# Kernel tuning notes

Hardware: AMD Instinct MI355X
Metric: run time of the kernel (lower is better)

## Reference

```python
import jax, jax.numpy as jnp
import numpy as np
from jax import lax

RATIOS = (0.5, 1.0, 2.0)
SCALES = (8, 16, 32)
BASE = 16
STRIDE = 16
N_PRE = 6000
N_POST = 300      # post-NMS proposals kept
NMS_THRESH = 0.7
MIN_SIZE = 16.0


def _anchor_base():
    x = y = BASE / 2.0
    ab = np.zeros((len(RATIOS) * len(SCALES), 4), np.float32)
    for i, r in enumerate(RATIOS):
        for j, s in enumerate(SCALES):
            h = BASE * s * np.sqrt(r)
            w = BASE * s * np.sqrt(1.0 / r)
            k = i * len(SCALES) + j
            ab[k] = [y - h / 2, x - w / 2, y + h / 2, x + w / 2]
    return ab


def _anchors(h, w):
    ab = _anchor_base()
    sy = np.arange(0, h * STRIDE, STRIDE)
    sx = np.arange(0, w * STRIDE, STRIDE)
    sx, sy = np.meshgrid(sx, sy)
    shift = np.stack((sy.ravel(), sx.ravel(), sy.ravel(), sx.ravel()), axis=1)
    # [K, A, 4] -> [K*A, 4], row-major over (y, x) pixels matching NHWC flatten
    return (ab[None, :, :] + shift[:, None, :]).reshape(-1, 4).astype(np.float32)


def _conv(x, w, b, pad):
    y = lax.conv_general_dilated(x, w, (1, 1), ((pad, pad), (pad, pad)),
                                 dimension_numbers=('NCHW', 'OIHW', 'NCHW'))
    return y + b[None, :, None, None]


def _loc2bbox(anchor, loc):
    h = anchor[:, 2] - anchor[:, 0]
    w = anchor[:, 3] - anchor[:, 1]
    cy = anchor[:, 0] + 0.5 * h
    cx = anchor[:, 1] + 0.5 * w
    dy, dx, dh, dw = loc[:, 0], loc[:, 1], loc[:, 2], loc[:, 3]
    ncy = dy * h + cy
    ncx = dx * w + cx
    nh = jnp.exp(dh) * h
    nw = jnp.exp(dw) * w
    return jnp.stack([ncy - 0.5 * nh, ncx - 0.5 * nw, ncy + 0.5 * nh, ncx + 0.5 * nw], axis=1)


def _iou(b):
    tl = jnp.maximum(b[:, None, :2], b[None, :, :2])
    br = jnp.minimum(b[:, None, 2:], b[None, :, 2:])
    wh = jnp.clip(br - tl, 0.0)
    inter = wh[..., 0] * wh[..., 1]
    area = (b[:, 2] - b[:, 0]) * (b[:, 3] - b[:, 1])
    return inter / (area[:, None] + area[None, :] - inter + 1e-9)


def _nms_keep(iou):
    # greedy NMS over score-sorted boxes: suppress later boxes overlapping kept earlier ones
    n = iou.shape[0]
    idx = jnp.arange(n)
    def step(keep, i):
        sup = (iou[i] > NMS_THRESH) & (idx > i) & keep[i]
        return keep & (~sup), None
    keep, _ = lax.scan(step, jnp.ones((n,), dtype=bool), idx)
    return keep


def _proposal(loc, fg, anchor, img_h, img_w, scale=1.0):
    boxes = _loc2bbox(anchor, loc)
    boxes = jnp.stack([jnp.clip(boxes[:, 0], 0.0, img_h),
                       jnp.clip(boxes[:, 1], 0.0, img_w),
                       jnp.clip(boxes[:, 2], 0.0, img_h),
                       jnp.clip(boxes[:, 3], 0.0, img_w)], axis=1)
    hs = boxes[:, 2] - boxes[:, 0]
    ws = boxes[:, 3] - boxes[:, 1]
    ms = MIN_SIZE * scale
    score = jnp.where((hs >= ms) & (ws >= ms), fg, -jnp.inf)
    top, idx = lax.top_k(score, N_PRE)
    bk = boxes[idx]                                    # [N_PRE, 4]
    keep = _nms_keep(_iou(lax.stop_gradient(bk)))      # selection is non-differentiable
    fs = jnp.where(keep, top, -jnp.inf)
    _, o2 = lax.top_k(fs, N_POST)
    return bk[o2]                                      # [N_POST, 4]


def setup_inputs() -> dict:
    key = jax.random.key(0)
    ks = jax.random.split(key, 4)
    C, H, W = 512, 50, 76
    return {
        "feature": jax.random.normal(ks[0], (1, C, H, W), jnp.float32),
        "conv1_w": jax.random.normal(ks[1], (512, C, 3, 3), jnp.float32) * 0.01,
        "conv1_b": jnp.zeros((512,), jnp.float32),
        "score_w": jax.random.normal(ks[2], (18, 512, 1, 1), jnp.float32) * 0.01,
        "score_b": jnp.zeros((18,), jnp.float32),
        "loc_w": jax.random.normal(ks[3], (36, 512, 1, 1), jnp.float32) * 0.01,
        "loc_b": jnp.zeros((36,), jnp.float32),
        "img_h": 800,
        "img_w": 1216,
    }


def reference(feature, conv1_w, conv1_b, score_w, score_b, loc_w, loc_b, img_h, img_w):
    _, c, h, w = feature.shape
    A = 9
    anchor = jnp.asarray(_anchors(h, w))
    x = jax.nn.relu(_conv(feature, conv1_w, conv1_b, 1))
    locs = _conv(x, loc_w, loc_b, 0)
    rpn_locs = locs.transpose(0, 2, 3, 1).reshape(1, -1, 4)
    sc = _conv(x, score_w, score_b, 0).transpose(0, 2, 3, 1)   # [1, h, w, 2A]
    sm = jax.nn.softmax(sc.reshape(1, h, w, A, 2), axis=-1)
    fg = sm[..., 1].reshape(-1)
    rpn_scores = sc.reshape(1, -1, 2)
    rois = _proposal(rpn_locs[0], fg, anchor, float(img_h), float(img_w), scale=1.0)
    return rpn_locs, rpn_scores, rois, anchor
```

## Files before the change

kernel.cpp:

```cpp
#include <hip/hip_runtime.h>

#define HH 50
#define WW2 76
#define NPIX 3800
#define CIN 512
#define NANCH 34200
#define NPRE 6000
#define NPOST 300
#define WPR 94

typedef unsigned long long u64;
typedef unsigned int u32;

__device__ __forceinline__ int PADL(int i) { return i + (i >> 4); }

template <bool DOW>
__global__ __launch_bounds__(256) void rpn_wtrans(const float* __restrict__ wgt,
                                                  float* __restrict__ wt,
                                                  const float* __restrict__ sw,
                                                  const float* __restrict__ lw,
                                                  float* __restrict__ wt2,
                                                  u32* __restrict__ hist,
                                                  u32* __restrict__ info) {
    __shared__ float tile[32][33];
    const int bx = blockIdx.x;
    const int by = blockIdx.y;
    const int t  = threadIdx.x;
    const int tx = t & 31, ty = t >> 5;
    int gid = (by * 144 + bx) * 256 + t;
    if (gid < 65536) hist[gid] = 0u;
    else if (gid < 65552) info[gid - 65536] = 0u;
    if (gid < 32768) {
        int c = gid >> 6, n = gid & 63;
        float v = 0.f;
        if (n < 18) v = sw[n * 512 + c];
        else if (n < 54) v = lw[(n - 18) * 512 + c];
        wt2[((c >> 2) * 64 + n) * 4 + (c & 3)] = v;
    }
    if (!DOW) return;
#pragma unroll
    for (int r = 0; r < 32; r += 8) {
        int ko = by * 32 + ty + r;
        tile[ty + r][tx] = wgt[(size_t)ko * 4608 + bx * 32 + tx];
    }
    __syncthreads();
#pragma unroll
    for (int r = 0; r < 32; r += 8) {
        int cit = bx * 32 + ty + r;
        wt[(size_t)cit * 512 + by * 32 + tx] = tile[tx][ty + r];
    }
}

template <bool USEWT>
__global__ __launch_bounds__(256, 2) void rpn_conv1(
    const float* __restrict__ feat, const float* __restrict__ wsrc,
    float* __restrict__ Xpt, int cin_blk, int czbase) {
    const int yb = blockIdx.x;
    const int kg = blockIdx.y;
    const int cz = blockIdx.z + czbase;
    const int t  = threadIdx.x;
    const int kp = t & 15;
    const int ty = t >> 4;
    const int row  = ty >> 2;
    const int xseg = ty & 3;
    const int x0 = xseg * 19;
    __shared__ float in_l[2048];
    __shared__ float w_l[2304];

    const int y0 = yb * 4 - 1;
    int inSrc[8]; u32 inValid = 0, inPad = 0;
#pragma unroll
    for (int k = 0; k < 8; ++k) {
        int q = t + k * 256;
        int c = q / 504, rem = q - c * 504;
        int r = rem / 84, xx = rem - r * 84;
        int gy = y0 + r, gx = xx - 1;
        bool inb = q < 2016;
        bool ok = inb && ((unsigned)gy < 50u) && ((unsigned)gx < 76u);
        inSrc[k] = c * NPIX + gy * 76 + gx;
        if (ok) inValid |= (1u << k);
        else if (inb) inPad |= (1u << k);
    }
#pragma unroll
    for (int k = 0; k < 8; ++k)
        if ((inPad >> k) & 1) in_l[t + k * 256] = 0.f;

    const float* wb;
    int wOffA = 0;
    int wSrc[9];
    if (USEWT) {
        wb = wsrc + (size_t)(cz * cin_blk) * 9 * 512 + kg * 64;
        wOffA = 8 * t - 7 * (t & 63);
    } else {
        wb = wsrc + (size_t)(kg * 64) * 4608 + (size_t)(cz * cin_blk) * 9;
#pragma unroll
        for (int k = 0; k < 9; ++k) {
            int q = t + k * 256;
            int c = q / 576, r2 = q - c * 576;
            int tap = r2 >> 6, ko = r2 & 63;
            wSrc[k] = ko * 4608 + c * 9 + tap;
        }
    }

    const float* fb = feat + (size_t)(cz * cin_blk) * NPIX;
    float acc[4][19];
#pragma unroll
    for (int o = 0; o < 4; ++o)
#pragma unroll
        for (int p = 0; p < 19; ++p) acc[o][p] = 0.f;

    const int niter = cin_blk >> 2;
#pragma unroll 1
    for (int it = 0; it < niter; ++it) {
        __syncthreads();
#pragma unroll
        for (int k = 0; k < 8; ++k)
            if ((inValid >> k) & 1) in_l[t + k * 256] = fb[inSrc[k]];
        if (USEWT) {
#pragma unroll
            for (int k = 0; k < 9; ++k)
                w_l[t + k * 256] = wb[wOffA + k * 2048];
        } else {
#pragma unroll
            for (int k = 0; k < 9; ++k)
                w_l[t + k * 256] = wb[wSrc[k]];
        }
        __syncthreads();
#pragma unroll 1
        for (int c = 0; c < 4; ++c) {
            const float* ir0 = &in_l[(c * 6 + row) * 84 + x0];
            const float* wl  = &w_l[c * 576 + 4 * kp];
#pragma unroll
            for (int r = 0; r < 3; ++r) {
                const float* ir = ir0 + r * 84;
                float win[21];
#pragma unroll
                for (int w = 0; w < 21; ++w) win[w] = ir[w];
                float wv[4][3];
#pragma unroll
                for (int tp = 0; tp < 3; ++tp) {
                    const float* wr = wl + (r * 3 + tp) * 64;
#pragma unroll
                    for (int o = 0; o < 4; ++o) wv[o][tp] = wr[o];
                }
#pragma unroll
                for (int p = 0; p < 19; ++p) {
#pragma unroll
                    for (int o = 0; o < 4; ++o) {
                        acc[o][p] = fmaf(wv[o][0], win[p],     acc[o][p]);
                        acc[o][p] = fmaf(wv[o][1], win[p + 1], acc[o][p]);
                        acc[o][p] = fmaf(wv[o][2], win[p + 2], acc[o][p]);
                    }
                }
            }
        }
        fb += 4 * NPIX;
        wb += USEWT ? 4 * 9 * 512 : 36;
    }

    const int k0 = kg * 64 + 4 * kp;
    const int y = yb * 4 + row;
    if (y < 50) {
        float* d0 = Xpt + ((size_t)cz * NPIX + y * 76 + x0) * 512 + k0;
#pragma unroll
        for (int p = 0; p < 19; ++p)
            *reinterpret_cast<float4*>(d0 + (size_t)p * 512) =
                make_float4(acc[0][p], acc[1][p], acc[2][p], acc[3][p]);
    }
}

__global__ __launch_bounds__(256) void rpn_head(
    const float* __restrict__ Xpt, const float* __restrict__ wt2,
    const float* __restrict__ b1,
    const float* __restrict__ sb, const float* __restrict__ lb,
    const int* __restrict__ ihp, const int* __restrict__ iwp,
    float* __restrict__ out, float* __restrict__ boxes,
    u32* __restrict__ keys, u32* __restrict__ hist, int nz) {
    const int p0 = blockIdx.x * 8;
    const int t  = threadIdx.x;
    __shared__ __align__(16) float xs[8 * 512];
    __shared__ float ovl[8][64];
    float4* dst = reinterpret_cast<float4*>(xs);
#pragma unroll
    for (int i = 0; i < 4; ++i) {
        int idx = t + i * 256;
        int px = idx >> 7, cc = idx & 127;
        float4 v = *reinterpret_cast<const float4*>(b1 + cc * 4);
        const float* src = Xpt + ((size_t)(p0 + px)) * 512 + cc * 4;
        for (int z = 0; z < nz; ++z) {
            float4 x = *reinterpret_cast<const float4*>(src + (size_t)z * NPIX * 512);
            v.x += x.x; v.y += x.y; v.z += x.z; v.w += x.w;
        }
        v.x = fmaxf(v.x, 0.f); v.y = fmaxf(v.y, 0.f);
        v.z = fmaxf(v.z, 0.f); v.w = fmaxf(v.w, 0.f);
        dst[idx] = v;
    }
    __syncthreads();
    const int w = t >> 6, lane = t & 63;
    float a0, a1;
    {
        float b = (lane < 18) ? sb[lane] : ((lane < 54) ? lb[lane - 18] : 0.f);
        a0 = b; a1 = b;
    }
    const float4* wv = reinterpret_cast<const float4*>(wt2) + lane;
    const float* x0b = xs + (2 * w) * 512;
    const float* x1b = xs + (2 * w + 1) * 512;
#pragma unroll 4
    for (int c4 = 0; c4 < 128; ++c4) {
        float4 wq = wv[c4 * 64];
        float4 xa = *reinterpret_cast<const float4*>(x0b + c4 * 4);
        float4 xb = *reinterpret_cast<const float4*>(x1b + c4 * 4);
        a0 = fmaf(wq.x, xa.x, a0); a0 = fmaf(wq.y, xa.y, a0);
        a0 = fmaf(wq.z, xa.z, a0); a0 = fmaf(wq.w, xa.w, a0);
        a1 = fmaf(wq.x, xb.x, a1); a1 = fmaf(wq.y, xb.y, a1);
        a1 = fmaf(wq.z, xb.z, a1); a1 = fmaf(wq.w, xb.w, a1);
    }
    if (lane < 54) { ovl[2 * w][lane] = a0; ovl[2 * w + 1][lane] = a1; }
    __syncthreads();
    if (t < 72) {
        const int px = t / 9, a = t - px * 9;
        const float ch = (float)(*ihp), cw = (float)(*iwp);
        const int p = p0 + px;
        const float* ov = ovl[px];
        const float s0 = ov[2 * a], s1 = ov[2 * a + 1];
        const float dy = ov[18 + 4 * a], dx = ov[18 + 4 * a + 1];
        const float dh = ov[18 + 4 * a + 2], dw = ov[18 + 4 * a + 3];
        const int yy = p / WW2, xx = p % WW2;
        const int ai = p * 9 + a;
        *reinterpret_cast<float4*>(out + ai * 4) = make_float4(dy, dx, dh, dw);
        *reinterpret_cast<float2*>(out + 136800 + ai * 2) = make_float2(s0, s1);
        double r  = (a < 3) ? 0.5 : (a < 6) ? 1.0 : 2.0;
        int m3 = a % 3;
        double s2 = (m3 == 0) ? 8.0 : (m3 == 1) ? 16.0 : 32.0;
        double hd = (16.0 * s2) * sqrt(r);
        double wd = (16.0 * s2) * sqrt(1.0 / r);
        float ay1 = (float)(8.0 - hd * 0.5), ax1 = (float)(8.0 - wd * 0.5);
        float ay2 = (float)(8.0 + hd * 0.5), ax2 = (float)(8.0 + wd * 0.5);
        float fy = (float)(yy * 16), fx = (float)(xx * 16);
        float A0 = ay1 + fy, A1 = ax1 + fx, A2 = ay2 + fy, A3 = ax2 + fx;
        *reinterpret_cast<float4*>(out + 206400 + ai * 4) = make_float4(A0, A1, A2, A3);
        float ah = __fsub_rn(A2, A0), aw = __fsub_rn(A3, A1);
        float cy = __fadd_rn(A0, __fmul_rn(0.5f, ah));
        float cx = __fadd_rn(A1, __fmul_rn(0.5f, aw));
        float ncy = __fadd_rn(__fmul_rn(dy, ah), cy);
        float ncx = __fadd_rn(__fmul_rn(dx, aw), cx);
        float nh = __fmul_rn(expf(dh), ah);
        float nw = __fmul_rn(expf(dw), aw);
        float b0 = __fsub_rn(ncy, __fmul_rn(0.5f, nh));
        float b1v = __fsub_rn(ncx, __fmul_rn(0.5f, nw));
        float b2 = __fadd_rn(ncy, __fmul_rn(0.5f, nh));
        float b3 = __fadd_rn(ncx, __fmul_rn(0.5f, nw));
        b0 = fminf(fmaxf(b0, 0.f), ch); b2 = fminf(fmaxf(b2, 0.f), ch);
        b1v = fminf(fmaxf(b1v, 0.f), cw); b3 = fminf(fmaxf(b3, 0.f), cw);
        float hs = __fsub_rn(b2, b0), wsz = __fsub_rn(b3, b1v);
        float m = fmaxf(s0, s1);
        float e0 = expf(__fsub_rn(s0, m)), e1 = expf(__fsub_rn(s1, m));
        float fg = __fdiv_rn(e1, __fadd_rn(e0, e1));
        float score = (hs >= 16.f && wsz >= 16.f) ? fg : -__builtin_inff();
        *reinterpret_cast<float4*>(boxes + ai * 4) = make_float4(b0, b1v, b2, b3);
        u32 kb = __float_as_uint(score);
        kb = (kb & 0x80000000u) ? ~kb : (kb | 0x80000000u);
        keys[ai] = kb;
        atomicAdd(&hist[kb >> 16], 1u);
    }
}

__global__ __launch_bounds__(1024) void rpn_threshsel(const u32* __restrict__ hist,
                                                      u32* __restrict__ info,
                                                      const u32* __restrict__ keys,
                                                      u64* __restrict__ selk) {
    __shared__ u32 tmp[1024];
    __shared__ u32 part[256], h2[256];
    __shared__ int segs;
    __shared__ u32 Tsh;
    const int t = threadIdx.x;
    {
        u32 s = 0;
        const u32* hp = hist + t * 64;
#pragma unroll 8
        for (int b = 0; b < 64; ++b) s += hp[b];
        tmp[t] = s;
    }
    __syncthreads();
    if (t < 256) part[t] = tmp[4 * t] + tmp[4 * t + 1] + tmp[4 * t + 2] + tmp[4 * t + 3];
    __syncthreads();
    for (int off = 1; off < 256; off <<= 1) {
        u32 v = 0, add = 0;
        if (t < 256) { v = part[t]; add = (t + off < 256) ? part[t + off] : 0u; }
        __syncthreads();
        if (t < 256) part[t] = v + add;
        __syncthreads();
    }
    if (t < 256) {
        u32 suf  = part[t];
        u32 sufn = (t < 255) ? part[t + 1] : 0u;
        if (suf >= NPRE && sufn < NPRE) segs = t;
    }
    __syncthreads();
    const int seg = segs;
    const u32 above = (seg < 255) ? part[seg + 1] : 0u;
    if (t < 256) h2[t] = hist[seg * 256 + t];
    __syncthreads();
    for (int off = 1; off < 256; off <<= 1) {
        u32 v = 0, add = 0;
        if (t < 256) { v = h2[t]; add = (t + off < 256) ? h2[t + off] : 0u; }
        __syncthreads();
        if (t < 256) h2[t] = v + add;
        __syncthreads();
    }
    if (t < 256) {
        u32 tot  = above + h2[t];
        u32 totn = above + ((t < 255) ? h2[t + 1] : 0u);
        if (tot >= NPRE && totn < NPRE) Tsh = (u32)(seg * 256 + t);
    }
    __syncthreads();
    const u32 T = Tsh;
    const int lane = t & 63;
    for (int base = 0; base < NANCH; base += 1024) {
        int idx = base + t;
        u32 k = (idx < NANCH) ? keys[idx] : 0u;
        bool sel = (idx < NANCH) && ((k >> 16) >= T);
        u64 ball = __ballot(sel);
        u32 wbase = 0;
        if (lane == 0 && ball) wbase = atomicAdd(&info[2], (u32)__popcll(ball));
        wbase = __shfl(wbase, 0);
        if (sel) {
            u32 pos = wbase + (u32)__popcll(ball & ((1ull << lane) - 1ull));
            if (pos < 8192) selk[pos] = ((u64)k << 32) | (u64)(0xFFFFFFFFu - (u32)idx);
        }
    }
}

__global__ __launch_bounds__(1024) void rpn_sort_local(u64* __restrict__ selk,
                                                       const u32* __restrict__ info) {
    __shared__ u64 s[2176];
    const int t = threadIdx.x;
    const int seg = blockIdx.x;
    const int base = seg * 2048;
    int n = (int)info[2]; if (n > 8192) n = 8192;
    for (int i = t; i < 2048; i += 1024)
        s[PADL(i)] = (base + i < n) ? selk[base + i] : 0ull;
    __syncthreads();
    const bool D = ((seg & 1) == 0);
    for (int k = 2; k <= 2048; k <<= 1) {
        for (int j = k >> 1; j > 0; j >>= 1) {
            int p1 = ((t & ~(j - 1)) << 1) | (t & (j - 1));
            int p2 = p1 | j;
            bool desc = (((p1 & k) == 0) == D);
            u64 A = s[PADL(p1)], B = s[PADL(p2)];
            if (desc ? (A < B) : (A > B)) { s[PADL(p1)] = B; s[PADL(p2)] = A; }
            __syncthreads();
        }
    }
    for (int i = t; i < 2048; i += 1024) selk[base + i] = s[PADL(i)];
}

__global__ __launch_bounds__(512) void rpn_sort_gpass(u64* __restrict__ selk,
                                                      int k, int j) {
    int i = blockIdx.x * 512 + threadIdx.x;
    int p1 = ((i & ~(j - 1)) << 1) | (i & (j - 1));
    int p2 = p1 | j;
    bool desc = ((p1 & k) == 0);
    u64 A = selk[p1], B = selk[p2];
    if (desc ? (A < B) : (A > B)) { selk[p1] = B; selk[p2] = A; }
}

template <bool FINAL>
__global__ __launch_bounds__(1024) void rpn_sort_lmerge(u64* __restrict__ selk, int k,
                                                        const float* __restrict__ boxes,
                                                        float* __restrict__ bk) {
    __shared__ u64 s[2176];
    const int t = threadIdx.x;
    const int base = blockIdx.x * 2048;
    for (int i = t; i < 2048; i += 1024) s[PADL(i)] = selk[base + i];
    __syncthreads();
    const bool desc = ((base & k) == 0);
    for (int j = 1024; j > 0; j >>= 1) {
        int p1 = ((t & ~(j - 1)) << 1) | (t & (j - 1));
        int p2 = p1 | j;
        u64 A = s[PADL(p1)], B = s[PADL(p2)];
        if (desc ? (A < B) : (A > B)) { s[PADL(p1)] = B; s[PADL(p2)] = A; }
        __syncthreads();
    }
    if (FINAL) {
        for (int i = t; i < 2048; i += 1024) {
            int r = base + i;
            if (r < NPRE) {
                u32 oi = 0xFFFFFFFFu - (u32)(s[PADL(i)] & 0xFFFFFFFFull);
                if (oi >= NANCH) oi = 0;
                reinterpret_cast<float4*>(bk)[r] = reinterpret_cast<const float4*>(boxes)[oi];
            }
        }
    } else {
        for (int i = t; i < 2048; i += 1024) selk[base + i] = s[PADL(i)];
    }
}

__global__ __launch_bounds__(256) void rpn_iou(const float* __restrict__ bk,
                                               u64* __restrict__ mask) {
    const int t = threadIdx.x;
    const int lane = t & 63, w = t >> 6;
    const int bj = blockIdx.x;
    const int bi = blockIdx.y * 4 + w;
    const int j0 = bj * 64;
    __shared__ float4 jb[64];
    if (t < 64) jb[t] = (j0 + t < NPRE) ? reinterpret_cast<const float4*>(bk)[j0 + t]
                                        : make_float4(0.f, 0.f, 0.f, 0.f);
    __syncthreads();
    if (bi >= WPR) return;
    const int i = bi * 64 + lane;
    if (j0 + 63 <= bi * 64) {
        if (i < NPRE) mask[(size_t)i * WPR + bj] = 0ull;
        return;
    }
    if (i >= NPRE) return;
    float4 b = reinterpret_cast<const float4*>(bk)[i];
    float areai = __fmul_rn(__fsub_rn(b.z, b.x), __fsub_rn(b.w, b.y));
    u64 bits = 0ull;
    for (int jj = 0; jj < 64; ++jj) {
        int j = j0 + jj;
        if (j <= i || j >= NPRE) continue;
        float4 c = jb[jj];
        float ty = fmaxf(b.x, c.x), tx = fmaxf(b.y, c.y);
        float by = fminf(b.z, c.z), bx2 = fminf(b.w, c.w);
        float ih = fmaxf(__fsub_rn(by, ty), 0.f);
        float iw = fmaxf(__fsub_rn(bx2, tx), 0.f);
        float inter = __fmul_rn(ih, iw);
        float areaj = __fmul_rn(__fsub_rn(c.z, c.x), __fsub_rn(c.w, c.y));
        float denom = __fadd_rn(__fsub_rn(__fadd_rn(areai, areaj), inter), 1e-9f);
        float iou = __fdiv_rn(inter, denom);
        if (iou > 0.7f) bits |= (1ull << jj);
    }
    mask[(size_t)i * WPR + bj] = bits;
}

__global__ __launch_bounds__(64) void rpn_nms(const u64* __restrict__ mask,
                                              const float* __restrict__ bk,
                                              float* __restrict__ rois) {
    const int lane = threadIdx.x;
    u64 rem0 = 0ull, rem1 = 0ull, curW = 0ull;
    __shared__ unsigned short klist[304];
    int kcnt = 0;
    u64 pm0[16], pm1[16], pmg[16];
#pragma unroll
    for (int u = 0; u < 16; ++u) {
        pm0[u] = mask[(size_t)u * WPR + lane];
        pm1[u] = (lane < 30) ? mask[(size_t)u * WPR + 64 + lane] : 0ull;
        pmg[u] = mask[(size_t)u * WPR + 0];
    }
    bool done = false;
    for (int base = 0; base < NPRE && !done; base += 16) {
        if ((base & 63) == 0) {
            int w = base >> 6;
            curW = (w < 64) ? __shfl(rem0, w) : __shfl(rem1, w - 64);
        }
#pragma unroll
        for (int u = 0; u < 16; ++u) {
            const int i = base + u;
            u64 m0 = pm0[u], m1 = pm1[u], mg = pmg[u];
            const int ni = i + 16;
            pm0[u] = mask[(size_t)ni * WPR + lane];
            pm1[u] = (lane < 30) ? mask[(size_t)ni * WPR + 64 + lane] : 0ull;
            pmg[u] = mask[(size_t)ni * WPR + (ni >> 6)];
            if (((curW >> (i & 63)) & 1ull) == 0ull) {
                rem0 |= m0;
                rem1 |= m1;
                curW |= mg;
                if (lane == 0 && kcnt < 304) klist[kcnt] = (unsigned short)i;
                ++kcnt;
                if (kcnt >= NPOST) { done = true; break; }
            }
        }
    }
    __syncthreads();
    const int nk = kcnt < NPOST ? kcnt : NPOST;
    for (int r = lane; r < nk; r += 64) {
        int bi = klist[r];
        reinterpret_cast<float4*>(rois)[r] = reinterpret_cast<const float4*>(bk)[bi];
    }
    if (kcnt < NPOST) {
        int pos = kcnt;
        for (int i = 0; i < NPRE && pos < NPOST; ++i) {
            int w = i >> 6;
            u64 wv = (w < 64) ? __shfl(rem0, w) : __shfl(rem1, w - 64);
            if ((wv >> (i & 63)) & 1ull) {
                if (lane < 4) rois[pos * 4 + lane] = bk[i * 4 + lane];
                ++pos;
            }
        }
    }
}

extern "C" void kernel_launch(void* const* d_in, const int* in_sizes, int n_in,
                              void* d_out, int out_size, void* d_ws, size_t ws_size,
                              hipStream_t stream) {
    (void)in_sizes; (void)n_in; (void)out_size;
    const float* feat = (const float*)d_in[0];
    const float* w1   = (const float*)d_in[1];
    const float* b1   = (const float*)d_in[2];
    const float* sw   = (const float*)d_in[3];
    const float* sb   = (const float*)d_in[4];
    const float* lw   = (const float*)d_in[5];
    const float* lb   = (const float*)d_in[6];
    const int*   ih   = (const int*)d_in[7];
    const int*   iw   = (const int*)d_in[8];
    float* out = (float*)d_out;

    const size_t WT_B    = 9437184;
    const size_t WT2_B   = 131072;
    const size_t REST_B  = WT2_B + 547200 + 136800 + 262144 + 64 + 65536 + 96000 + 4528128;
    const size_t SLICE_B = (size_t)512 * NPIX * 4;
    int nz; bool usewt;
    if      (ws_size >= 8 * SLICE_B + WT_B + REST_B) { nz = 8; usewt = true; }
    else if (ws_size >= 4 * SLICE_B + WT_B + REST_B) { nz = 4; usewt = true; }
    else if (ws_size >= 2 * SLICE_B + WT_B + REST_B) { nz = 2; usewt = true; }
    else                                             { nz = 2; usewt = false; }

    char* p = (char*)d_ws;
    float* Xpt = (float*)p;          p += (size_t)nz * SLICE_B;
    float* wt = nullptr;
    if (usewt) { wt = (float*)p;     p += WT_B; }
    float* wt2    = (float*)p;       p += WT2_B;
    float* boxes  = (float*)p;       p += 547200;
    u32*   keys   = (u32*)p;         p += 136800;
    u32*   hist   = (u32*)p;         p += 262144;
    u32*   info   = (u32*)p;         p += 64;
    u64*   selk   = (u64*)p;         p += 65536;
    float* bk     = (float*)p;       p += 96000;
    u64*   mask   = (u64*)p;

    const int cin_blk = 512 / nz;

    if (usewt) {
        rpn_wtrans<true><<<dim3(144, 16), 256, 0, stream>>>(w1, wt, sw, lw, wt2, hist, info);
        rpn_conv1<true><<<dim3(13, 8, nz), 256, 0, stream>>>(feat, wt, Xpt, cin_blk, 0);
    } else {
        rpn_wtrans<false><<<dim3(144, 16), 256, 0, stream>>>(w1, nullptr, sw, lw, wt2, hist, info);
        rpn_conv1<false><<<dim3(13, 8, nz), 256, 0, stream>>>(feat, w1, Xpt, cin_blk, 0);
    }
    rpn_head<<<475, 256, 0, stream>>>(Xpt, wt2, b1, sb, lb, ih, iw, out, boxes, keys, hist, nz);
    rpn_threshsel<<<1, 1024, 0, stream>>>(hist, info, keys, selk);
    rpn_sort_local<<<4, 1024, 0, stream>>>(selk, info);
    rpn_sort_gpass<<<8, 512, 0, stream>>>(selk, 4096, 2048);
    rpn_sort_lmerge<false><<<4, 1024, 0, stream>>>(selk, 4096, nullptr, nullptr);
    rpn_sort_gpass<<<8, 512, 0, stream>>>(selk, 8192, 4096);
    rpn_sort_gpass<<<8, 512, 0, stream>>>(selk, 8192, 2048);
    rpn_sort_lmerge<true><<<4, 1024, 0, stream>>>(selk, 8192, boxes, bk);
    rpn_iou<<<dim3(WPR, 24), 256, 0, stream>>>(bk, mask);
    rpn_nms<<<1, 64, 0, stream>>>(mask, bk, out + 205200);
}
```

Baseline: 575.5 us.

## Split threshold/select into separate kernels and deepen NMS mask prefetch to 64 rows

The single-block threshold-and-select kernel becomes a 256-thread threshold kernel plus a grid-wide select kernel. The selection scan over all anchors is then spread across many blocks instead of being looped by one block. The NMS kernel's register prefetch pipeline grows from 16 to 64 mask rows, so the serial greedy loop waits less on memory. The workspace mask size is enlarged to cover the deeper prefetch past the last row. The trade-offs are an extra kernel launch and much higher register pressure (192 u64 arrays per lane) in NMS, which could spill.

```diff
diff --git a/kernel.cpp b/kernel.cpp
--- a/kernel.cpp
+++ b/kernel.cpp
@@ -265,69 +265,56 @@
     }
 }
 
-__global__ __launch_bounds__(1024) void rpn_threshsel(const u32* __restrict__ hist,
-                                                      u32* __restrict__ info,
-                                                      const u32* __restrict__ keys,
-                                                      u64* __restrict__ selk) {
-    __shared__ u32 tmp[1024];
+__global__ __launch_bounds__(256) void rpn_thresh(const u32* __restrict__ hist,
+                                                  u32* __restrict__ info) {
     __shared__ u32 part[256], h2[256];
     __shared__ int segs;
-    __shared__ u32 Tsh;
     const int t = threadIdx.x;
-    {
-        u32 s = 0;
-        const u32* hp = hist + t * 64;
-#pragma unroll 8
-        for (int b = 0; b < 64; ++b) s += hp[b];
-        tmp[t] = s;
-    }
-    __syncthreads();
-    if (t < 256) part[t] = tmp[4 * t] + tmp[4 * t + 1] + tmp[4 * t + 2] + tmp[4 * t + 3];
+    u32 s = 0;
+    const u32* hp = hist + t * 256;
+    for (int b = 0; b < 256; ++b) s += hp[b];
+    part[t] = s;
     __syncthreads();
     for (int off = 1; off < 256; off <<= 1) {
-        u32 v = 0, add = 0;
-        if (t < 256) { v = part[t]; add = (t + off < 256) ? part[t + off] : 0u; }
-        __syncthreads();
-        if (t < 256) part[t] = v + add;
-        __syncthreads();
-    }
-    if (t < 256) {
-        u32 suf  = part[t];
-        u32 sufn = (t < 255) ? part[t + 1] : 0u;
-        if (suf >= NPRE && sufn < NPRE) segs = t;
-    }
+        u32 v = part[t];
+        u32 add = (t + off < 256) ? part[t + off] : 0u;
+        __syncthreads();
+        part[t] = v + add;
+        __syncthreads();
+    }
+    u32 suf  = part[t];
+    u32 sufn = (t < 255) ? part[t + 1] : 0u;
+    if (suf >= NPRE && sufn < NPRE) segs = t;
     __syncthreads();
     const int seg = segs;
     const u32 above = (seg < 255) ? part[seg + 1] : 0u;
-    if (t < 256) h2[t] = hist[seg * 256 + t];
+    h2[t] = hist[seg * 256 + t];
     __syncthreads();
     for (int off = 1; off < 256; off <<= 1) {
-        u32 v = 0, add = 0;
-        if (t < 256) { v = h2[t]; add = (t + off < 256) ? h2[t + off] : 0u; }
-        __syncthreads();
-        if (t < 256) h2[t] = v + add;
-        __syncthreads();
-    }
-    if (t < 256) {
-        u32 tot  = above + h2[t];
-        u32 totn = above + ((t < 255) ? h2[t + 1] : 0u);
-        if (tot >= NPRE && totn < NPRE) Tsh = (u32)(seg * 256 + t);
-    }
-    __syncthreads();
-    const u32 T = Tsh;
-    const int lane = t & 63;
-    for (int base = 0; base < NANCH; base += 1024) {
-        int idx = base + t;
-        u32 k = (idx < NANCH) ? keys[idx] : 0u;
-        bool sel = (idx < NANCH) && ((k >> 16) >= T);
-        u64 ball = __ballot(sel);
-        u32 wbase = 0;
-        if (lane == 0 && ball) wbase = atomicAdd(&info[2], (u32)__popcll(ball));
-        wbase = __shfl(wbase, 0);
-        if (sel) {
-            u32 pos = wbase + (u32)__popcll(ball & ((1ull << lane) - 1ull));
-            if (pos < 8192) selk[pos] = ((u64)k << 32) | (u64)(0xFFFFFFFFu - (u32)idx);
-        }
+        u32 v = h2[t];
+        u32 add = (t + off < 256) ? h2[t + off] : 0u;
+        __syncthreads();
+        h2[t] = v + add;
+        __syncthreads();
+    }
+    u32 tot  = above + h2[t];
+    u32 totn = above + ((t < 255) ? h2[t + 1] : 0u);
+    if (tot >= NPRE && totn < NPRE) info[0] = (u32)(seg * 256 + t);
+}
+
+__global__ void rpn_select(const u32* __restrict__ keys, u32* __restrict__ info,
+                           u64* __restrict__ selk) {
+    const int idx = blockIdx.x * 256 + threadIdx.x;
+    const int lane = threadIdx.x & 63;
+    u32 k = (idx < NANCH) ? keys[idx] : 0u;
+    bool sel = (idx < NANCH) && ((k >> 16) >= info[0]);
+    u64 ball = __ballot(sel);
+    u32 base = 0;
+    if (lane == 0 && ball) base = atomicAdd(&info[2], (u32)__popcll(ball));
+    base = __shfl(base, 0);
+    if (sel) {
+        u32 pos = base + (u32)__popcll(ball & ((1ull << lane) - 1ull));
+        if (pos < 8192) selk[pos] = ((u64)k << 32) | (u64)(0xFFFFFFFFu - (u32)idx);
     }
 }
 
@@ -434,31 +421,31 @@
     mask[(size_t)i * WPR + bj] = bits;
 }
 
-__global__ __launch_bounds__(64) void rpn_nms(const u64* __restrict__ mask,
-                                              const float* __restrict__ bk,
-                                              float* __restrict__ rois) {
+__global__ __launch_bounds__(64, 1) void rpn_nms(const u64* __restrict__ mask,
+                                                 const float* __restrict__ bk,
+                                                 float* __restrict__ rois) {
     const int lane = threadIdx.x;
     u64 rem0 = 0ull, rem1 = 0ull, curW = 0ull;
     __shared__ unsigned short klist[304];
     int kcnt = 0;
-    u64 pm0[16], pm1[16], pmg[16];
-#pragma unroll
-    for (int u = 0; u < 16; ++u) {
+    u64 pm0[64], pm1[64], pmg[64];
+#pragma unroll
+    for (int u = 0; u < 64; ++u) {
         pm0[u] = mask[(size_t)u * WPR + lane];
         pm1[u] = (lane < 30) ? mask[(size_t)u * WPR + 64 + lane] : 0ull;
-        pmg[u] = mask[(size_t)u * WPR + 0];
+        pmg[u] = mask[(size_t)u * WPR + (u >> 6)];
     }
     bool done = false;
-    for (int base = 0; base < NPRE && !done; base += 16) {
-        if ((base & 63) == 0) {
+    for (int base = 0; base < NPRE && !done; base += 64) {
+        {
             int w = base >> 6;
             curW = (w < 64) ? __shfl(rem0, w) : __shfl(rem1, w - 64);
         }
 #pragma unroll
-        for (int u = 0; u < 16; ++u) {
+        for (int u = 0; u < 64; ++u) {
             const int i = base + u;
             u64 m0 = pm0[u], m1 = pm1[u], mg = pmg[u];
-            const int ni = i + 16;
+            const int ni = i + 64;
             pm0[u] = mask[(size_t)ni * WPR + lane];
             pm1[u] = (lane < 30) ? mask[(size_t)ni * WPR + 64 + lane] : 0ull;
             pmg[u] = mask[(size_t)ni * WPR + (ni >> 6)];
@@ -508,7 +495,8 @@
 
     const size_t WT_B    = 9437184;
     const size_t WT2_B   = 131072;
-    const size_t REST_B  = WT2_B + 547200 + 136800 + 262144 + 64 + 65536 + 96000 + 4528128;
+    const size_t MASK_B  = 4580000;
+    const size_t REST_B  = WT2_B + 547200 + 136800 + 262144 + 64 + 65536 + 96000 + MASK_B;
     const size_t SLICE_B = (size_t)512 * NPIX * 4;
     int nz; bool usewt;
     if      (ws_size >= 8 * SLICE_B + WT_B + REST_B) { nz = 8; usewt = true; }
@@ -539,7 +527,8 @@
         rpn_conv1<false><<<dim3(13, 8, nz), 256, 0, stream>>>(feat, w1, Xpt, cin_blk, 0);
     }
     rpn_head<<<475, 256, 0, stream>>>(Xpt, wt2, b1, sb, lb, ih, iw, out, boxes, keys, hist, nz);
-    rpn_threshsel<<<1, 1024, 0, stream>>>(hist, info, keys, selk);
+    rpn_thresh<<<1, 256, 0, stream>>>(hist, info);
+    rpn_select<<<(NANCH + 255) / 256, 256, 0, stream>>>(keys, info, selk);
     rpn_sort_local<<<4, 1024, 0, stream>>>(selk, info);
     rpn_sort_gpass<<<8, 512, 0, stream>>>(selk, 4096, 2048);
     rpn_sort_lmerge<false><<<4, 1024, 0, stream>>>(selk, 4096, nullptr, nullptr);
```

New measurement: 671.6 us. 16.7% more time.
